# Kernel optimization log

Measured on AMD Instinct MI355X. Metric: run time of the kernel, lower is better.

Reference implementation:

```python
import jax, jax.numpy as jnp
import numpy as np

P = 16          # patch size
IMG = 224       # image size
EPS_COMBINE = 2.220446049250313e-16  # np.finfo(float).eps
NOISE_EPS = 0.01
LOSS_COEF = 1e-2
K = 1


def _patchify(x):
    # x: [B, C, H, W] -> [B, n_patches, C*P*P] (channel-major flatten, matching conv weight layout)
    B, C, H, W = x.shape
    gh, gw = H // P, W // P
    x = x.reshape(B, C, gh, P, gw, P)
    x = x.transpose(0, 2, 4, 1, 3, 5).reshape(B, gh * gw, C * P * P)
    return x


def _cv_squared(v):
    # squared coefficient of variation; torch .var() is unbiased (ddof=1)
    return jnp.var(v, ddof=1) / (jnp.mean(v) ** 2 + 1e-10)


def _norm_cdf(v):
    return jax.scipy.stats.norm.cdf(v)


def setup_inputs() -> dict:
    key = jax.random.key(0)
    ks = jax.random.split(key, 7)
    B, E, D_IN = 64, 8, 320
    x = jax.random.normal(ks[0], (B, 3, IMG, IMG), dtype=jnp.float32)
    g = jax.random.normal(ks[1], (B, D_IN), dtype=jnp.float32)
    noise = jax.random.normal(ks[2], (B, E), dtype=jnp.float32)
    w_gate = jax.random.normal(ks[3], (D_IN, E), dtype=jnp.float32) * 0.02
    w_noise = jax.random.normal(ks[4], (D_IN, E), dtype=jnp.float32) * 0.02
    w_exp = jax.random.normal(ks[5], (E, 768, 3, P, P), dtype=jnp.float32) * 0.02
    b_exp = jnp.zeros((E, 768), dtype=jnp.float32)
    return {"x": x, "g": g, "noise": noise, "w_gate": w_gate,
            "w_noise": w_noise, "w_exp": w_exp, "b_exp": b_exp}


def reference(x, g, noise, w_gate, w_noise, w_exp, b_exp):
    B = x.shape[0]
    E = w_gate.shape[1]

    # ---- noisy top-k gating (train mode) ----
    clean_logits = g @ w_gate                                   # [B, E]
    noise_stddev = jax.nn.softplus(g @ w_noise) + NOISE_EPS     # [B, E]
    noisy_logits = clean_logits + noise * noise_stddev          # [B, E]

    top_logits, top_idx = jax.lax.top_k(noisy_logits, K + 1)    # [B, K+1]
    top_k_gates = jax.nn.softmax(top_logits[:, :K], axis=1)     # [B, K]
    gates = jnp.zeros_like(noisy_logits).at[
        jnp.arange(B)[:, None], top_idx[:, :K]].set(top_k_gates)  # [B, E]

    # load: prob each expert's noisy logit lands in top-k (differentiable balance term)
    thr_in = top_logits[:, K][:, None]       # (k+1)-th value per row
    thr_out = top_logits[:, K - 1][:, None]  # k-th value per row
    is_in = noisy_logits > thr_in
    prob = jnp.where(is_in,
                     _norm_cdf((clean_logits - thr_in) / noise_stddev),
                     _norm_cdf((clean_logits - thr_out) / noise_stddev))
    load = prob.sum(0)                                           # [E]
    importance = gates.sum(0)                                    # [E]
    loss = (_cv_squared(importance) + _cv_squared(load)) * LOSS_COEF

    # ---- experts: per-expert patch-embed conv == patchify + GEMM ----
    patches = _patchify(x)                                       # [B, 196, 768]
    wf = w_exp.reshape(E, w_exp.shape[1], -1)                    # [E, out=768, in=768]
    y_exp = jnp.einsum('bpi,eoi->ebpo', patches, wf) + b_exp[:, None, None, :]  # [E,B,196,768]

    # ---- gate-weighted combine (dense equivalent of dispatch/combine) ----
    y = jnp.einsum('be,ebpo->bpo', gates, y_exp)                 # [B, 196, 768]
    y = jnp.where(y == 0, jnp.asarray(EPS_COMBINE, y.dtype), y)  # combined[combined==0] = eps
    return y, loss
```

## Files before the change

kernel.cpp:

```cpp
#include <hip/hip_runtime.h>
#include <math.h>

typedef unsigned short u16;
typedef unsigned int   u32;

using bf16x8 = __attribute__((ext_vector_type(8))) short;
using f32x4  = __attribute__((ext_vector_type(4))) float;

#define NB   64
#define NE   8
#define DIN  320
#define NP   196
#define CK   768
#define CN   768
#define NKT  24

#define GATE_BLOCKS  8
#define WPACK_BLOCKS 2304
#define APACK_BLOCKS 1024

__device__ __forceinline__ u16 f2bf(float f) {
    u32 u = __builtin_bit_cast(u32, f);
    u += 0x7fffu + ((u >> 16) & 1u);
    return (u16)(u >> 16);
}

__global__ __launch_bounds__(256) void prep1_kernel(
    const float* __restrict__ x,
    const float* __restrict__ g,
    const float* __restrict__ noise,
    const float* __restrict__ w_gate,
    const float* __restrict__ w_noise,
    const float* __restrict__ w_exp,
    float* __restrict__ gCl, float* __restrict__ gSd, float* __restrict__ gNy,
    u16* __restrict__ apk,
    u16* __restrict__ wpk)
{
    __shared__ char smem[24704];
    const int t = threadIdx.x;
    int bid = blockIdx.x;

    if (bid < GATE_BLOCKS) {
        float (*sW)[NE + 1]  = (float (*)[NE + 1])smem;
        float (*sWn)[NE + 1] = sW + DIN;
        for (int i = t; i < DIN * NE; i += 256) {
            sW[i >> 3][i & 7]  = w_gate[i];
            sWn[i >> 3][i & 7] = w_noise[i];
        }
        __syncthreads();
        const int pair = t >> 2, q = t & 3;
        const int bl = pair >> 3, e = pair & 7;
        const int b = bid * 8 + bl;
        float cl = 0.f, nz = 0.f;
        const float* gr = g + b * DIN + q * 80;
        #pragma unroll 4
        for (int j = 0; j < 80; ++j) {
            float gv = gr[j];
            cl = fmaf(gv, sW[q * 80 + j][e], cl);
            nz = fmaf(gv, sWn[q * 80 + j][e], nz);
        }
        cl += __shfl_xor(cl, 1); cl += __shfl_xor(cl, 2);
        nz += __shfl_xor(nz, 1); nz += __shfl_xor(nz, 2);
        if (q == 0) {
            int p = b * NE + e;
            float sd = fmaxf(nz, 0.f) + log1pf(expf(-fabsf(nz))) + 0.01f;
            gCl[p] = cl; gSd[p] = sd;
            gNy[p] = fmaf(noise[p], sd, cl);
        }
        return;
    }
    bid -= GATE_BLOCKS;

    if (bid < WPACK_BLOCKS) {
        int idx = bid * 256 + t;
        int chunk = idx >> 6, l = idx & 63;
        int e   = chunk / 1152;
        int rem = chunk % 1152;
        int fnG = rem / 24;
        int kb  = rem % 24;
        const float* src = w_exp + ((size_t)(e * CN + fnG * 16 + (l & 15))) * CK
                         + kb * 32 + (l >> 4) * 8;
        float4 f0 = *reinterpret_cast<const float4*>(src);
        float4 f1 = *reinterpret_cast<const float4*>(src + 4);
        uint4 o;
        o.x = (u32)f2bf(f0.x) | ((u32)f2bf(f0.y) << 16);
        o.y = (u32)f2bf(f0.z) | ((u32)f2bf(f0.w) << 16);
        o.z = (u32)f2bf(f1.x) | ((u32)f2bf(f1.y) << 16);
        o.w = (u32)f2bf(f1.z) | ((u32)f2bf(f1.w) << 16);
        *reinterpret_cast<uint4*>(wpk + (size_t)chunk * 512 + l * 8) = o;
        return;
    }
    bid -= WPACK_BLOCKS;

    {
        char* pk = smem;
        const int b  = bid >> 4;
        const int fr = bid & 15;
        #pragma unroll
        for (int s = 0; s < 3; ++s) {
            int u  = t + s * 256;
            int lr = u / 48;
            int c  = (u >> 4) % 3;
            int ph = u & 15;
            int p  = fr * 16 + lr; if (p > NP - 1) p = NP - 1;
            const float* src = x + ((size_t)(b * 3 + c) * 224 + (p / 14) * 16 + ph) * 224
                                 + (p % 14) * 16;
            float4 f0 = *reinterpret_cast<const float4*>(src);
            float4 f1 = *reinterpret_cast<const float4*>(src + 4);
            float4 f2 = *reinterpret_cast<const float4*>(src + 8);
            float4 f3 = *reinterpret_cast<const float4*>(src + 12);
            uint4 o0, o1;
            o0.x = (u32)f2bf(f0.x) | ((u32)f2bf(f0.y) << 16);
            o0.y = (u32)f2bf(f0.z) | ((u32)f2bf(f0.w) << 16);
            o0.z = (u32)f2bf(f1.x) | ((u32)f2bf(f1.y) << 16);
            o0.w = (u32)f2bf(f1.z) | ((u32)f2bf(f1.w) << 16);
            o1.x = (u32)f2bf(f2.x) | ((u32)f2bf(f2.y) << 16);
            o1.y = (u32)f2bf(f2.z) | ((u32)f2bf(f2.w) << 16);
            o1.z = (u32)f2bf(f3.x) | ((u32)f2bf(f3.y) << 16);
            o1.w = (u32)f2bf(f3.z) | ((u32)f2bf(f3.w) << 16);
            u32 base = (u32)((c * 8 + (ph >> 1)) * 1024 + ((ph & 1) * 2) * 256 + lr * 16);
            *reinterpret_cast<uint4*>(pk + base)       = o0;
            *reinterpret_cast<uint4*>(pk + base + 256) = o1;
        }
        __syncthreads();
        char* dst = (char*)apk + ((size_t)(b * 16 + fr) * 24) * 1024;
        #pragma unroll
        for (int s = 0; s < 6; ++s)
            *reinterpret_cast<uint4*>(dst + t * 16 + s * 4096) =
                *reinterpret_cast<const uint4*>(pk + t * 16 + s * 4096);
    }
}

__global__ __launch_bounds__(512) void gate2_kernel(
    const float* __restrict__ gCl,
    const float* __restrict__ gSd,
    const float* __restrict__ gNy,
    int* __restrict__ eid,
    int* __restrict__ perm,
    float* __restrict__ loss_out)
{
    __shared__ float sNy[NB][NE];
    __shared__ float sProb[NB][NE];
    __shared__ int   sTop[NB];
    __shared__ float sImp[NE], sLoad[NE];
    const int t = threadIdx.x;
    const int b = t >> 3, e = t & 7;
    float cl = gCl[t], sd = gSd[t], ny = gNy[t];
    sNy[b][e] = ny;
    __syncthreads();
    float v1 = -1e30f, v2 = -1e30f; int i1 = 0;
    #pragma unroll
    for (int k2 = 0; k2 < NE; ++k2) {
        float v = sNy[b][k2];
        if (v > v1) { v2 = v1; v1 = v; i1 = k2; }
        else if (v > v2) { v2 = v; }
    }
    if (e == 0) { sTop[b] = i1; eid[b] = i1; }
    float thr = (ny > v2) ? v2 : v1;
    float z = (cl - thr) / sd;
    sProb[b][e] = 0.5f * (1.0f + erff(z * 0.7071067811865476f));
    __syncthreads();
    if (t < NE) {
        float imp = 0.f, ld = 0.f;
        for (int i = 0; i < NB; ++i) {
            imp += (sTop[i] == t) ? 1.0f : 0.0f;
            ld  += sProb[i][t];
        }
        sImp[t] = imp; sLoad[t] = ld;
    }
    __syncthreads();
    if (t == 0) {
        float mi = 0.f, ml = 0.f;
        for (int k2 = 0; k2 < NE; ++k2) { mi += sImp[k2]; ml += sLoad[k2]; }
        mi *= (1.0f / NE); ml *= (1.0f / NE);
        float vi = 0.f, vl = 0.f;
        for (int k2 = 0; k2 < NE; ++k2) {
            float d1 = sImp[k2] - mi;  vi += d1 * d1;
            float d2 = sLoad[k2] - ml; vl += d2 * d2;
        }
        vi *= (1.0f / (NE - 1)); vl *= (1.0f / (NE - 1));
        loss_out[0] = (vi / (mi * mi + 1e-10f) + vl / (ml * ml + 1e-10f)) * 0.01f;
        int off[NE]; int s = 0;
        #pragma unroll
        for (int k2 = 0; k2 < NE; ++k2) { off[k2] = s; s += (int)sImp[k2]; }
        for (int i = 0; i < NB; ++i) perm[off[sTop[i]]++] = i;
    }
}

__global__ __launch_bounds__(256) void gemm_kernel(
    const u16* __restrict__ apk,
    const u16* __restrict__ wpk,
    const float* __restrict__ b_exp,
    const int* __restrict__ eid,
    const int* __restrict__ perm,
    float* __restrict__ out)
{
    const int id = blockIdx.x;
    const int v  = (id & 7) * 96 + (id >> 3);
    const int b  = perm[v / 12];
    const int rr = v % 12;
    const int mt = rr / 6;
    const int nt = rr % 6;
    const int e  = eid[b];

    const int t  = threadIdx.x;
    const int l  = t & 63;
    const int w  = t >> 6;
    const int wm = w >> 1;
    const int wn = w & 1;

    const char* aB[4];
    const char* bB[4];
    #pragma unroll
    for (int fm = 0; fm < 4; ++fm)
        aB[fm] = (const char*)apk
               + ((size_t)((b * 16 + mt * 8 + wm * 4 + fm) * 24)) * 1024 + l * 16;
    #pragma unroll
    for (int fn = 0; fn < 4; ++fn)
        bB[fn] = (const char*)wpk
               + ((size_t)((e * 48 + nt * 8 + wn * 4 + fn) * 24)) * 1024 + l * 16;

    f32x4 acc[4][4];
    #pragma unroll
    for (int fm = 0; fm < 4; ++fm)
        #pragma unroll
        for (int fn = 0; fn < 4; ++fn)
            acc[fm][fn] = (f32x4){0.f, 0.f, 0.f, 0.f};

    bf16x8 a0[4], b0[4], a1[4], b1[4], a2[4], b2[4];

    auto LD = [&](bf16x8 (&ra)[4], bf16x8 (&rb)[4], int k) {
        if (k > NKT - 1) k = NKT - 1;
        #pragma unroll
        for (int f = 0; f < 4; ++f) {
            ra[f] = *reinterpret_cast<const bf16x8*>(aB[f] + k * 1024);
            rb[f] = *reinterpret_cast<const bf16x8*>(bB[f] + k * 1024);
        }
    };
    auto MM = [&](bf16x8 (&ra)[4], bf16x8 (&rb)[4]) {
        __builtin_amdgcn_s_setprio(1);
        #pragma unroll
        for (int fm = 0; fm < 4; ++fm)
            #pragma unroll
            for (int fn = 0; fn < 4; ++fn)
                acc[fm][fn] = __builtin_amdgcn_mfma_f32_16x16x32_bf16(
                    ra[fm], rb[fn], acc[fm][fn], 0, 0, 0);
        __builtin_amdgcn_s_setprio(0);
    };

    LD(a0, b0, 0);
    LD(a1, b1, 1);

    #pragma unroll 1
    for (int gq = 0; gq < 8; ++gq) {
        const int k3 = 3 * gq;
        LD(a2, b2, k3 + 2); MM(a0, b0);
        LD(a0, b0, k3 + 3); MM(a1, b1);
        LD(a1, b1, k3 + 4); MM(a2, b2);
    }

    const int r4 = (l >> 4) * 4;
    #pragma unroll
    for (int fm = 0; fm < 4; ++fm) {
        int mb = mt * 128 + wm * 64 + fm * 16 + r4;
        #pragma unroll
        for (int fn = 0; fn < 4; ++fn) {
            int col = nt * 128 + wn * 64 + fn * 16 + (l & 15);
            float bias = b_exp[e * CN + col];
            #pragma unroll
            for (int q = 0; q < 4; ++q) {
                int mrow = mb + q;
                if (mrow < NP) {
                    float vv = acc[fm][fn][q] + bias;
                    if (vv == 0.0f) vv = 2.220446049250313e-16f;
                    out[((size_t)b * NP + mrow) * CN + col] = vv;
                }
            }
        }
    }
}

extern "C" void kernel_launch(void* const* d_in, const int* in_sizes, int n_in,
                              void* d_out, int out_size, void* d_ws, size_t ws_size,
                              hipStream_t stream) {
    const float* x       = (const float*)d_in[0];
    const float* g       = (const float*)d_in[1];
    const float* noise   = (const float*)d_in[2];
    const float* w_gate  = (const float*)d_in[3];
    const float* w_noise = (const float*)d_in[4];
    const float* w_exp   = (const float*)d_in[5];
    const float* b_exp   = (const float*)d_in[6];
    float* out = (float*)d_out;

    char* ws = (char*)d_ws;
    int*   eid  = (int*)ws;
    int*   perm = (int*)(ws + 256);
    float* gCl  = (float*)(ws + 512);
    float* gSd  = (float*)(ws + 2560);
    float* gNy  = (float*)(ws + 4608);
    u16*   apk  = (u16*)(ws + 8192);
    u16*   wpk  = (u16*)(ws + 8192 + (size_t)64 * 16 * 24 * 1024);

    hipLaunchKernelGGL(prep1_kernel,
                       dim3(GATE_BLOCKS + WPACK_BLOCKS + APACK_BLOCKS), dim3(256), 0, stream,
                       x, g, noise, w_gate, w_noise, w_exp, gCl, gSd, gNy, apk, wpk);
    hipLaunchKernelGGL(gate2_kernel, dim3(1), dim3(512), 0, stream,
                       gCl, gSd, gNy, eid, perm, out + (size_t)NB * NP * CN);
    hipLaunchKernelGGL(gemm_kernel, dim3(768), dim3(256), 0, stream,
                       apk, wpk, b_exp, eid, perm, out);
}
```

Measured before the change: 67.50 us.

## Group GEMM by expert with LDS-resident weight slices and per-expert batch loops

The expert GEMM is reorganised so each block owns one expert and one 96-column weight slice. It loads that whole slice (96x768 bf16) into shared memory once with global_load_lds and then loops over all batch items routed to that expert, using per-expert offsets computed in the gating kernel. Each half of the 512-thread block processes a different batch item, with A fragments streamed from global memory. This removes repeated weight fetches across tiles, but it needs 144KB of LDS (one block per CU) and only 192 blocks, so a skewed expert distribution can leave work unbalanced across CUs.

Result: slower. 85.48 us (+26.6%).

```diff
diff --git a/kernel.cpp b/kernel.cpp
--- a/kernel.cpp
+++ b/kernel.cpp
@@ -23,6 +23,12 @@
     u32 u = __builtin_bit_cast(u32, f);
     u += 0x7fffu + ((u >> 16) & 1u);
     return (u16)(u >> 16);
+}
+
+__device__ __forceinline__ void gload16(const void* g, void* l) {
+    __builtin_amdgcn_global_load_lds(
+        (const __attribute__((address_space(1))) void*)g,
+        (__attribute__((address_space(3))) void*)l, 16, 0, 0);
 }
 
 __global__ __launch_bounds__(256) void prep1_kernel(
@@ -135,8 +141,8 @@
     const float* __restrict__ gCl,
     const float* __restrict__ gSd,
     const float* __restrict__ gNy,
-    int* __restrict__ eid,
     int* __restrict__ perm,
+    int* __restrict__ offs,
     float* __restrict__ loss_out)
 {
     __shared__ float sNy[NB][NE];
@@ -155,7 +161,7 @@
         if (v > v1) { v2 = v1; v1 = v; i1 = k2; }
         else if (v > v2) { v2 = v; }
     }
-    if (e == 0) { sTop[b] = i1; eid[b] = i1; }
+    if (e == 0) sTop[b] = i1;
     float thr = (ny > v2) ? v2 : v1;
     float z = (cl - thr) / sd;
     sProb[b][e] = 0.5f * (1.0f + erff(z * 0.7071067811865476f));
@@ -180,100 +186,119 @@
         }
         vi *= (1.0f / (NE - 1)); vl *= (1.0f / (NE - 1));
         loss_out[0] = (vi / (mi * mi + 1e-10f) + vl / (ml * ml + 1e-10f)) * 0.01f;
-        int off[NE]; int s = 0;
-        #pragma unroll
-        for (int k2 = 0; k2 < NE; ++k2) { off[k2] = s; s += (int)sImp[k2]; }
-        for (int i = 0; i < NB; ++i) perm[off[sTop[i]]++] = i;
-    }
-}
-
-__global__ __launch_bounds__(256) void gemm_kernel(
+        int off[NE + 1]; off[0] = 0;
+        #pragma unroll
+        for (int k2 = 0; k2 < NE; ++k2) off[k2 + 1] = off[k2] + (int)sImp[k2];
+        #pragma unroll
+        for (int k2 = 0; k2 <= NE; ++k2) offs[k2] = off[k2];
+        int cur[NE];
+        #pragma unroll
+        for (int k2 = 0; k2 < NE; ++k2) cur[k2] = off[k2];
+        for (int i = 0; i < NB; ++i) perm[cur[sTop[i]]++] = i;
+    }
+}
+
+__global__ void __launch_bounds__(512, 2) gemm_kernel(
     const u16* __restrict__ apk,
     const u16* __restrict__ wpk,
     const float* __restrict__ b_exp,
-    const int* __restrict__ eid,
     const int* __restrict__ perm,
+    const int* __restrict__ offs,
     float* __restrict__ out)
 {
-    const int id = blockIdx.x;
-    const int v  = (id & 7) * 96 + (id >> 3);
-    const int b  = perm[v / 12];
-    const int rr = v % 12;
-    const int mt = rr / 6;
-    const int nt = rr % 6;
-    const int e  = eid[b];
+    extern __shared__ char sB[];
+
+    const int id  = blockIdx.x;
+    const int e   = id & 7;
+    const int nt  = (id >> 3) & 7;
+    const int grp = id >> 6;
+
+    const int beg = offs[e] + grp;
+    const int end = offs[e + 1];
+    if (beg >= end) return;
 
     const int t  = threadIdx.x;
     const int l  = t & 63;
     const int w  = t >> 6;
-    const int wm = w >> 1;
-    const int wn = w & 1;
-
-    const char* aB[4];
-    const char* bB[4];
-    #pragma unroll
-    for (int fm = 0; fm < 4; ++fm)
-        aB[fm] = (const char*)apk
-               + ((size_t)((b * 16 + mt * 8 + wm * 4 + fm) * 24)) * 1024 + l * 16;
-    #pragma unroll
-    for (int fn = 0; fn < 4; ++fn)
-        bB[fn] = (const char*)wpk
-               + ((size_t)((e * 48 + nt * 8 + wn * 4 + fn) * 24)) * 1024 + l * 16;
-
-    f32x4 acc[4][4];
-    #pragma unroll
-    for (int fm = 0; fm < 4; ++fm)
-        #pragma unroll
-        for (int fn = 0; fn < 4; ++fn)
-            acc[fm][fn] = (f32x4){0.f, 0.f, 0.f, 0.f};
-
-    bf16x8 a0[4], b0[4], a1[4], b1[4], a2[4], b2[4];
-
-    auto LD = [&](bf16x8 (&ra)[4], bf16x8 (&rb)[4], int k) {
-        if (k > NKT - 1) k = NKT - 1;
-        #pragma unroll
-        for (int f = 0; f < 4; ++f) {
-            ra[f] = *reinterpret_cast<const bf16x8*>(aB[f] + k * 1024);
-            rb[f] = *reinterpret_cast<const bf16x8*>(bB[f] + k * 1024);
-        }
-    };
-    auto MM = [&](bf16x8 (&ra)[4], bf16x8 (&rb)[4]) {
-        __builtin_amdgcn_s_setprio(1);
+    const int hw = w >> 2;
+    const int wq = w & 3;
+
+    {
+        const char* src = (const char*)wpk + ((size_t)(e * 48 + nt * 6) * 24) * 1024;
+        #pragma unroll
+        for (int s = 0; s < 18; ++s)
+            gload16(src + s * 8192 + t * 16, sB + s * 8192 + (w * 1024 + l * 16));
+    }
+    asm volatile("s_waitcnt vmcnt(0)" ::: "memory");
+    __syncthreads();
+
+    const u32 bl16 = (u32)(l * 16);
+    const int r4 = (l >> 4) * 4;
+
+    for (int i = beg; i < end; i += 6) {
+        const int  bA  = perm[i];
+        const bool has2 = (i + 3 < end);
+        const int  bI  = hw ? (has2 ? perm[i + 3] : bA) : bA;
+        const bool doSt = hw ? has2 : true;
+
+        const char* aBase = (const char*)apk
+                          + ((size_t)((bI * 16 + wq * 4) * 24)) * 1024 + l * 16;
+
+        f32x4 acc[4][6];
         #pragma unroll
         for (int fm = 0; fm < 4; ++fm)
             #pragma unroll
-            for (int fn = 0; fn < 4; ++fn)
-                acc[fm][fn] = __builtin_amdgcn_mfma_f32_16x16x32_bf16(
-                    ra[fm], rb[fn], acc[fm][fn], 0, 0, 0);
-        __builtin_amdgcn_s_setprio(0);
-    };
-
-    LD(a0, b0, 0);
-    LD(a1, b1, 1);
-
-    #pragma unroll 1
-    for (int gq = 0; gq < 8; ++gq) {
-        const int k3 = 3 * gq;
-        LD(a2, b2, k3 + 2); MM(a0, b0);
-        LD(a0, b0, k3 + 3); MM(a1, b1);
-        LD(a1, b1, k3 + 4); MM(a2, b2);
-    }
-
-    const int r4 = (l >> 4) * 4;
-    #pragma unroll
-    for (int fm = 0; fm < 4; ++fm) {
-        int mb = mt * 128 + wm * 64 + fm * 16 + r4;
-        #pragma unroll
-        for (int fn = 0; fn < 4; ++fn) {
-            int col = nt * 128 + wn * 64 + fn * 16 + (l & 15);
-            float bias = b_exp[e * CN + col];
-            #pragma unroll
-            for (int q = 0; q < 4; ++q) {
-                int mrow = mb + q;
-                if (mrow < NP) {
-                    float vv = acc[fm][fn][q] + bias;
-                    if (vv == 0.0f) vv = 2.220446049250313e-16f;
-                    out[((size_t)b * NP + mrow) * CN + col] = vv;
+            for (int j = 0; j < 6; ++j)
+                acc[fm][j] = (f32x4){0.f, 0.f, 0.f, 0.f};
+
+        bf16x8 aC[4], bC[6], aN[4], bN[6];
+
+        auto LDA = [&](bf16x8 (&ra)[4], bf16x8 (&rb)[6], int kb) {
+            if (kb > NKT - 1) kb = NKT - 1;
+            #pragma unroll
+            for (int fm = 0; fm < 4; ++fm)
+                ra[fm] = *reinterpret_cast<const bf16x8*>(aBase + (fm * 24 + kb) * 1024);
+            #pragma unroll
+            for (int j = 0; j < 6; ++j)
+                rb[j] = *reinterpret_cast<const bf16x8*>(sB + (u32)((j * 24 + kb) * 1024) + bl16);
+        };
+        auto MM = [&](bf16x8 (&ra)[4], bf16x8 (&rb)[6]) {
+            __builtin_amdgcn_s_setprio(1);
+            #pragma unroll
+            for (int fm = 0; fm < 4; ++fm)
+                #pragma unroll
+                for (int j = 0; j < 6; ++j)
+                    acc[fm][j] = __builtin_amdgcn_mfma_f32_16x16x32_bf16(
+                        ra[fm], rb[j], acc[fm][j], 0, 0, 0);
+            __builtin_amdgcn_s_setprio(0);
+        };
+
+        LDA(aC, bC, 0);
+        #pragma unroll 1
+        for (int kb = 0; kb < NKT; kb += 2) {
+            LDA(aN, bN, kb + 1);
+            MM(aC, bC);
+            LDA(aC, bC, kb + 2);
+            MM(aN, bN);
+        }
+
+        if (doSt) {
+            #pragma unroll
+            for (int fm = 0; fm < 4; ++fm) {
+                const int mb = wq * 64 + fm * 16 + r4;
+                #pragma unroll
+                for (int j = 0; j < 6; ++j) {
+                    const int col = nt * 96 + j * 16 + (l & 15);
+                    const float bias = b_exp[e * CN + col];
+                    #pragma unroll
+                    for (int q = 0; q < 4; ++q) {
+                        const int mrow = mb + q;
+                        if (mrow < NP) {
+                            float vv = acc[fm][j][q] + bias;
+                            if (vv == 0.0f) vv = 2.220446049250313e-16f;
+                            out[((size_t)bI * NP + mrow) * CN + col] = vv;
+                        }
+                    }
                 }
             }
         }
@@ -293,19 +318,22 @@
     float* out = (float*)d_out;
 
     char* ws = (char*)d_ws;
-    int*   eid  = (int*)ws;
-    int*   perm = (int*)(ws + 256);
+    int*   perm = (int*)ws;
+    int*   offs = (int*)(ws + 256);
     float* gCl  = (float*)(ws + 512);
     float* gSd  = (float*)(ws + 2560);
     float* gNy  = (float*)(ws + 4608);
     u16*   apk  = (u16*)(ws + 8192);
     u16*   wpk  = (u16*)(ws + 8192 + (size_t)64 * 16 * 24 * 1024);
 
+    hipFuncSetAttribute((const void*)gemm_kernel,
+                        hipFuncAttributeMaxDynamicSharedMemorySize, 147456);
+
     hipLaunchKernelGGL(prep1_kernel,
                        dim3(GATE_BLOCKS + WPACK_BLOCKS + APACK_BLOCKS), dim3(256), 0, stream,
                        x, g, noise, w_gate, w_noise, w_exp, gCl, gSd, gNy, apk, wpk);
     hipLaunchKernelGGL(gate2_kernel, dim3(1), dim3(512), 0, stream,
-                       gCl, gSd, gNy, eid, perm, out + (size_t)NB * NP * CN);
-    hipLaunchKernelGGL(gemm_kernel, dim3(768), dim3(256), 0, stream,
-                       apk, wpk, b_exp, eid, perm, out);
-}
+                       gCl, gSd, gNy, perm, offs, out + (size_t)NB * NP * CN);
+    hipLaunchKernelGGL(gemm_kernel, dim3(192), dim3(512), 147456, stream,
+                       apk, wpk, b_exp, perm, offs, out);
+}
```
